# Kernel optimization log

Measured on AMD Instinct MI355X. Metric: run time of the kernel, lower is better.

Reference implementation:

```python
import jax, jax.numpy as jnp
import numpy as np

B, C, CI, T, H, W = 2, 1024, 512, 32, 14, 14
N = T * H * W


def setup_inputs() -> dict:
    key = jax.random.key(0)
    ks = jax.random.split(key, 6)
    s_in = 1.0 / np.sqrt(C)
    s_mid = 1.0 / np.sqrt(CI)
    return {
        "x": jax.random.normal(ks[0], (B, C, T, H, W), jnp.float32),
        "Wk": jax.random.normal(ks[1], (CI, C), jnp.float32) * s_in,
        "bk": jnp.zeros((CI,), jnp.float32),
        "Wq": jax.random.normal(ks[2], (CI, C), jnp.float32) * s_in,
        "bq": jnp.zeros((CI,), jnp.float32),
        "Wv": jax.random.normal(ks[3], (CI, C), jnp.float32) * s_in,
        "bv": jnp.zeros((CI,), jnp.float32),
        "Wo": jax.random.normal(ks[4], (C, CI), jnp.float32) * s_mid,
        "bo": jnp.zeros((C,), jnp.float32),
    }


def reference(x, Wk, bk, Wq, bq, Wv, bv, Wo, bo):
    # x: (B, C, T, H, W). Dropout layers are identity at inference.
    b, c, t, h, w = x.shape
    n = t * h * w
    xf = x.reshape(b, c, n)                          # (B, C, N)
    k = jnp.einsum("dc,bcn->bdn", Wk, xf) + bk[None, :, None]   # (B, CI, N)
    q = jnp.einsum("dc,bcn->bdn", Wq, xf) + bq[None, :, None]   # (B, CI, N)
    v = jnp.einsum("dc,bcn->bdn", Wv, xf) + bv[None, :, None]   # (B, CI, N)
    # alpha[b,i,j] = sum_d key[b,i,d] * query[b,d,j], scaled by 1/T
    alpha = jnp.einsum("bdi,bdj->bij", k, q) / float(t)          # (B, N, N)
    alpha = jax.nn.softmax(alpha, axis=-1)
    # y (B, CI, N) with y[b,c,i] = sum_j alpha[b,i,j] * v[b,c,j]
    y = jnp.einsum("bij,bcj->bci", alpha, v)
    out = jnp.einsum("dc,bcn->bdn", Wo, y) + bo[None, :, None]   # (B, C, N)
    return out.reshape(b, c, t, h, w) + x
```

## Files before the change

kernel.cpp:

```cpp
#include <hip/hip_runtime.h>

#define Bb 2
#define Cc 1024
#define CIi 512
#define Nn 6272
#define JH 3136
#define SCALE (1.0f / 32.0f)

typedef __bf16 bf16;
typedef __bf16 bf16x8 __attribute__((ext_vector_type(8)));
typedef __bf16 bf16x4 __attribute__((ext_vector_type(4)));
typedef float f32x4 __attribute__((ext_vector_type(4)));
typedef float f32x2 __attribute__((ext_vector_type(2)));
typedef unsigned int u32;
typedef unsigned int u32x4 __attribute__((ext_vector_type(4)));

__device__ __forceinline__ void g2l16(const void* g, void* l) {
  __builtin_amdgcn_global_load_lds(
      (const __attribute__((address_space(1))) u32*)g,
      (__attribute__((address_space(3))) u32*)(size_t)l, 16, 0, 0);
}

__global__ __launch_bounds__(256) void xpose_kernel(const float* __restrict__ x,
                                                    bf16* __restrict__ xT) {
  __shared__ float tile[32][33];
  int b = blockIdx.z;
  int n0 = blockIdx.x * 32, c0 = blockIdx.y * 32;
  int tn = threadIdx.x & 31, tr = threadIdx.x >> 5;
  const float* xp = x + ((size_t)b * Cc + c0) * Nn + n0;
  for (int i = 0; i < 4; i++) {
    int c = tr + i * 8;
    tile[c][tn] = xp[(size_t)c * Nn + tn];
  }
  __syncthreads();
  bf16* op = xT + ((size_t)b * Nn + n0) * Cc + c0;
  for (int i = 0; i < 4; i++) {
    int n = tr + i * 8;
    op[(size_t)n * Cc + tn] = (bf16)tile[tn][n];
  }
}

__global__ __launch_bounds__(256) void proj_kernel(
    const bf16* __restrict__ xT, const float* __restrict__ Wk,
    const float* __restrict__ Wq, const float* __restrict__ Wv,
    const float* __restrict__ bk, const float* __restrict__ bq,
    const float* __restrict__ bv, bf16* __restrict__ kT, bf16* __restrict__ qT,
    bf16* __restrict__ vv) {
  int z = blockIdx.z;
  int b = z / 3, proj = z % 3;
  const float* W = proj == 0 ? Wk : (proj == 1 ? Wq : Wv);
  const float* bias = proj == 0 ? bk : (proj == 1 ? bq : bv);
  int m0 = blockIdx.x * 128;
  int d0 = blockIdx.y * 128;
  __shared__ __align__(16) bf16 la[128 * 40];
  __shared__ __align__(16) bf16 lb[128 * 40];
  int tid = threadIdx.x;
  int wave = tid >> 6, lane = tid & 63, quad = lane >> 4, l16 = lane & 15;
  int wm = (wave >> 1) * 64, wn = (wave & 1) * 64;
  int row2 = tid >> 1, half = tid & 1;

  f32x4 acc[4][4] = {};
  const bf16* aSrc = xT + ((size_t)b * Nn + m0) * Cc;
  const float* bSrc = W + (size_t)(d0 + row2) * Cc;

  for (int k0 = 0; k0 < Cc; k0 += 32) {
    const u32x4* ga = (const u32x4*)(aSrc + (size_t)row2 * Cc + k0 + half * 16);
    u32x4 a0 = ga[0], a1 = ga[1];
    const f32x4* gb = (const f32x4*)(bSrc + k0 + half * 16);
    f32x4 w0 = gb[0], w1 = gb[1], w2 = gb[2], w3 = gb[3];
    *(u32x4*)&la[row2 * 40 + half * 16] = a0;
    *(u32x4*)&la[row2 * 40 + half * 16 + 8] = a1;
    bf16x8 p0 = {(bf16)w0[0], (bf16)w0[1], (bf16)w0[2], (bf16)w0[3],
                 (bf16)w1[0], (bf16)w1[1], (bf16)w1[2], (bf16)w1[3]};
    bf16x8 p1 = {(bf16)w2[0], (bf16)w2[1], (bf16)w2[2], (bf16)w2[3],
                 (bf16)w3[0], (bf16)w3[1], (bf16)w3[2], (bf16)w3[3]};
    *(bf16x8*)&lb[row2 * 40 + half * 16] = p0;
    *(bf16x8*)&lb[row2 * 40 + half * 16 + 8] = p1;
    __syncthreads();
    bf16x8 af[4], bfr[4];
    for (int t = 0; t < 4; t++)
      af[t] = *(const bf16x8*)&la[(wm + t * 16 + l16) * 40 + quad * 8];
    for (int t = 0; t < 4; t++)
      bfr[t] = *(const bf16x8*)&lb[(wn + t * 16 + l16) * 40 + quad * 8];
    for (int tm = 0; tm < 4; tm++)
      for (int tn = 0; tn < 4; tn++)
        acc[tm][tn] = __builtin_amdgcn_mfma_f32_16x16x32_bf16(
            af[tm], bfr[tn], acc[tm][tn], 0, 0, 0);
    __syncthreads();
  }
  for (int tn = 0; tn < 4; tn++) {
    int dcol = d0 + wn + tn * 16 + l16;
    float bval = bias[dcol];
    for (int tm = 0; tm < 4; tm++) {
      int nbase = m0 + wm + tm * 16 + quad * 4;
      for (int r = 0; r < 4; r++) {
        float val = acc[tm][tn][r] + bval;
        int nrow = nbase + r;
        if (proj == 0) {
          kT[((size_t)b * Nn + nrow) * CIi + dcol] = (bf16)val;
        } else if (proj == 1) {
          int ch = (dcol >> 3) ^ (nrow & 7);
          qT[((size_t)b * Nn + nrow) * CIi + ch * 8 + (dcol & 7)] = (bf16)val;
        } else {
          vv[((size_t)b * CIi + dcol) * Nn + nrow] = (bf16)val;
        }
      }
    }
  }
}

__global__ __launch_bounds__(512, 2) void attn_kernel(
    const bf16* __restrict__ kT, const bf16* __restrict__ qTs,
    const bf16* __restrict__ vv, bf16* __restrict__ yp,
    float* __restrict__ ml) {
  int l = blockIdx.x;
  int jh = l & 1, b = (l >> 1) & 1;
  int i0 = (l >> 2) * 128;
  int tid = threadIdx.x;
  int wave = tid >> 6, lane = tid & 63, quad = lane >> 4, l16 = lane & 15;
  int dw = wave * 64;

  __shared__ __align__(16) bf16 lq[2][32 * 512];
  __shared__ __align__(16) bf16 Psm[128 * 36];
  __shared__ float red[128];

  const bf16* qb = qTs + ((size_t)b * Nn + (size_t)jh * JH) * CIi;
  const bf16* vb = vv + (size_t)b * CIi * Nn + (size_t)jh * JH;

  bf16x8 kf[16];
  {
    const bf16* kp =
        kT + ((size_t)b * Nn + i0 + wave * 16 + l16) * CIi + quad * 8;
#pragma unroll
    for (int kk = 0; kk < 16; kk++) kf[kk] = *(const bf16x8*)(kp + kk * 32);
  }
  f32x4 oacc[8][4] = {};
  f32x4 l_acc = {};

  {
    const bf16* qrow = qb + (size_t)(wave * 4) * CIi + lane * 8;
#pragma unroll
    for (int r = 0; r < 4; r++)
      g2l16(qrow + (size_t)r * CIi, &lq[0][(wave * 4 + r) * 512]);
  }
  __syncthreads();

  int x0 = l16 & 7;
  for (int j0 = 0; j0 < JH; j0 += 32) {
    int t = (j0 >> 5) & 1;
    if (j0 + 32 < JH) {
      const bf16* qrow = qb + (size_t)(j0 + 32 + wave * 4) * CIi + lane * 8;
#pragma unroll
      for (int r = 0; r < 4; r++)
        g2l16(qrow + (size_t)r * CIi, &lq[t ^ 1][(wave * 4 + r) * 512]);
    }
    f32x4 s0 = {}, s1 = {};
    {
      const bf16* q0 = &lq[t][l16 * 512];
      const bf16* q1 = &lq[t][(16 + l16) * 512];
#pragma unroll
      for (int kk = 0; kk < 16; kk++) {
        int ch = (((kk * 4 + quad) ^ x0)) * 8;
        bf16x8 qf0 = *(const bf16x8*)(q0 + ch);
        bf16x8 qf1 = *(const bf16x8*)(q1 + ch);
        s0 = __builtin_amdgcn_mfma_f32_16x16x32_bf16(kf[kk], qf0, s0, 0, 0, 0);
        s1 = __builtin_amdgcn_mfma_f32_16x16x32_bf16(kf[kk], qf1, s1, 0, 0, 0);
      }
    }
    {
#pragma unroll
      for (int r = 0; r < 4; r++) {
        float p0 = __expf(fminf(fmaf(s0[r], SCALE, -2.0f), 20.0f));
        float p1 = __expf(fminf(fmaf(s1[r], SCALE, -2.0f), 20.0f));
        l_acc[r] += p0 + p1;
        int gi = wave * 16 + quad * 4 + r;
        Psm[gi * 36 + l16] = (bf16)p0;
        Psm[gi * 36 + 16 + l16] = (bf16)p1;
      }
    }
    __syncthreads();

    {
      u32x4 vf[4];
#pragma unroll
      for (int ds = 0; ds < 4; ds++)
        vf[ds] = *(const u32x4*)(vb + (size_t)(dw + ds * 16 + l16) * Nn + j0 +
                                 quad * 8);
#pragma unroll
      for (int is = 0; is < 8; is++) {
        bf16x8 pf = *(const bf16x8*)&Psm[(is * 16 + l16) * 36 + quad * 8];
#pragma unroll
        for (int ds = 0; ds < 4; ds++)
          oacc[is][ds] = __builtin_amdgcn_mfma_f32_16x16x32_bf16(
              pf, __builtin_bit_cast(bf16x8, vf[ds]), oacc[is][ds], 0, 0, 0);
      }
    }
    __syncthreads();
  }

#pragma unroll
  for (int o = 1; o < 16; o <<= 1)
#pragma unroll
    for (int r = 0; r < 4; r++) l_acc[r] += __shfl_xor(l_acc[r], o);
  if (l16 == 0) {
#pragma unroll
    for (int r = 0; r < 4; r++) {
      int gi = wave * 16 + quad * 4 + r;
      ml[(size_t)(jh * Bb + b) * Nn + i0 + gi] = l_acc[r];
      red[gi] = 1.0f / l_acc[r];
    }
  }
  __syncthreads();
  bf16* ypb = yp + ((size_t)jh * Bb + b) * Nn * CIi;
#pragma unroll
  for (int is = 0; is < 8; is++) {
    f32x4 inv = *(const f32x4*)&red[is * 16 + quad * 4];
#pragma unroll
    for (int ds = 0; ds < 4; ds++)
#pragma unroll
      for (int r = 0; r < 4; r++)
        ypb[(size_t)(i0 + is * 16 + quad * 4 + r) * CIi + dw + ds * 16 + l16] =
            (bf16)(oacc[is][ds][r] * inv[r]);
  }
}

__global__ __launch_bounds__(256) void merge_kernel(const bf16* __restrict__ yp,
                                                    const float* __restrict__ ml,
                                                    bf16* __restrict__ y) {
  int idx = blockIdx.x * 256 + threadIdx.x;
  int row = idx >> 6, c = idx & 63;
  float l0 = ml[row];
  float l1 = ml[(size_t)Bb * Nn + row];
  float inv = 1.0f / (l0 + l1);
  float w0 = l0 * inv, w1 = l1 * inv;
  bf16x8 v0 = *(const bf16x8*)&yp[(size_t)row * CIi + c * 8];
  bf16x8 v1 =
      *(const bf16x8*)&yp[(size_t)Bb * Nn * CIi + (size_t)row * CIi + c * 8];
  bf16x8 o;
#pragma unroll
  for (int k = 0; k < 8; k++)
    o[k] = (bf16)(w0 * (float)v0[k] + w1 * (float)v1[k]);
  *(bf16x8*)&y[(size_t)row * CIi + c * 8] = o;
}

__global__ __launch_bounds__(256) void out_kernel(
    const bf16* __restrict__ y, const float* __restrict__ Wo,
    const float* __restrict__ bo, const float* __restrict__ x,
    float* __restrict__ out) {
  int b = blockIdx.z;
  int d0 = blockIdx.x * 128;
  int m0 = blockIdx.y * 128;
  __shared__ __align__(16) bf16 la[128 * 40];
  __shared__ __align__(16) bf16 lb[128 * 40];
  int tid = threadIdx.x;
  int wave = tid >> 6, lane = tid & 63, quad = lane >> 4, l16 = lane & 15;
  int wm = (wave >> 1) * 64, wn = (wave & 1) * 64;
  int row2 = tid >> 1, half = tid & 1;
  f32x4 acc[4][4] = {};
  const float* aSrc = Wo + (size_t)(d0 + row2) * CIi;
  const bf16* bSrc = y + ((size_t)b * Nn + m0 + row2) * CIi;
  for (int k0 = 0; k0 < CIi; k0 += 32) {
    const f32x4* ga = (const f32x4*)(aSrc + k0 + half * 16);
    f32x4 w0 = ga[0], w1 = ga[1], w2 = ga[2], w3 = ga[3];
    const u32x4* gb = (const u32x4*)(bSrc + k0 + half * 16);
    u32x4 b0 = gb[0], b1 = gb[1];
    bf16x8 p0 = {(bf16)w0[0], (bf16)w0[1], (bf16)w0[2], (bf16)w0[3],
                 (bf16)w1[0], (bf16)w1[1], (bf16)w1[2], (bf16)w1[3]};
    bf16x8 p1 = {(bf16)w2[0], (bf16)w2[1], (bf16)w2[2], (bf16)w2[3],
                 (bf16)w3[0], (bf16)w3[1], (bf16)w3[2], (bf16)w3[3]};
    *(bf16x8*)&la[row2 * 40 + half * 16] = p0;
    *(bf16x8*)&la[row2 * 40 + half * 16 + 8] = p1;
    *(u32x4*)&lb[row2 * 40 + half * 16] = b0;
    *(u32x4*)&lb[row2 * 40 + half * 16 + 8] = b1;
    __syncthreads();
    bf16x8 af[4], bfr[4];
    for (int t = 0; t < 4; t++)
      af[t] = *(const bf16x8*)&la[(wm + t * 16 + l16) * 40 + quad * 8];
    for (int t = 0; t < 4; t++)
      bfr[t] = *(const bf16x8*)&lb[(wn + t * 16 + l16) * 40 + quad * 8];
    for (int tm = 0; tm < 4; tm++)
      for (int tn = 0; tn < 4; tn++)
        acc[tm][tn] = __builtin_amdgcn_mfma_f32_16x16x32_bf16(
            af[tm], bfr[tn], acc[tm][tn], 0, 0, 0);
    __syncthreads();
  }
  for (int tm = 0; tm < 4; tm++) {
    for (int r = 0; r < 4; r++) {
      int drow = d0 + wm + tm * 16 + quad * 4 + r;
      float bval = bo[drow];
      const float* xrow = x + ((size_t)b * Cc + drow) * Nn;
      float* orow = out + ((size_t)b * Cc + drow) * Nn;
      for (int tn = 0; tn < 4; tn++) {
        int ncol = m0 + wn + tn * 16 + l16;
        orow[ncol] = acc[tm][tn][r] + bval + xrow[ncol];
      }
    }
  }
}

extern "C" void kernel_launch(void* const* d_in, const int* in_sizes, int n_in,
                              void* d_out, int out_size, void* d_ws,
                              size_t ws_size, hipStream_t stream) {
  (void)in_sizes;
  (void)n_in;
  (void)out_size;
  (void)ws_size;
  const float* x = (const float*)d_in[0];
  const float* Wk = (const float*)d_in[1];
  const float* bk = (const float*)d_in[2];
  const float* Wq = (const float*)d_in[3];
  const float* bq = (const float*)d_in[4];
  const float* Wv = (const float*)d_in[5];
  const float* bv = (const float*)d_in[6];
  const float* Wo = (const float*)d_in[7];
  const float* bo = (const float*)d_in[8];
  float* out = (float*)d_out;

  bf16* xT = (bf16*)d_ws;
  bf16* yp = (bf16*)d_ws;
  bf16* y = (bf16*)d_ws + (size_t)Bb * Nn * Cc;
  bf16* kT = (bf16*)d_out;
  bf16* qT = kT + (size_t)Bb * Nn * CIi;
  bf16* vv = qT + (size_t)Bb * Nn * CIi;
  float* ml = (float*)((char*)d_out + (size_t)40 * 1024 * 1024);

  xpose_kernel<<<dim3(Nn / 32, Cc / 32, Bb), 256, 0, stream>>>(x, xT);
  proj_kernel<<<dim3(Nn / 128, CIi / 128, 3 * Bb), 256, 0, stream>>>(
      xT, Wk, Wq, Wv, bk, bq, bv, kT, qT, vv);
  attn_kernel<<<dim3((Nn / 128) * 2 * Bb), 512, 0, stream>>>(kT, qT, vv, yp,
                                                             ml);
  merge_kernel<<<dim3(Bb * Nn * 64 / 256), 256, 0, stream>>>(yp, ml, y);
  out_kernel<<<dim3(Cc / 128, Nn / 128, Bb), 256, 0, stream>>>(y, Wo, bo, x,
                                                               out);
}
```

Before: 577.6 us.

## Widen attention j-tile to 64 with 2D wave split of QK^T

```diff
diff --git a/kernel.cpp b/kernel.cpp
--- a/kernel.cpp
+++ b/kernel.cpp
@@ -118,81 +118,100 @@
   int i0 = (l >> 2) * 128;
   int tid = threadIdx.x;
   int wave = tid >> 6, lane = tid & 63, quad = lane >> 4, l16 = lane & 15;
+  int wi = wave & 3, wj = wave >> 2;
   int dw = wave * 64;
 
-  __shared__ __align__(16) bf16 lq[2][32 * 512];
-  __shared__ __align__(16) bf16 Psm[128 * 36];
-  __shared__ float red[128];
+  __shared__ __align__(16) bf16 lq[2][64 * 512];
+  __shared__ __align__(16) bf16 Psm[128 * 64];
+  __shared__ __align__(16) float redw[2][128];
+  __shared__ __align__(16) float redi[128];
 
   const bf16* qb = qTs + ((size_t)b * Nn + (size_t)jh * JH) * CIi;
   const bf16* vb = vv + (size_t)b * CIi * Nn + (size_t)jh * JH;
 
-  bf16x8 kf[16];
+  bf16x8 kf[2][16];
   {
     const bf16* kp =
-        kT + ((size_t)b * Nn + i0 + wave * 16 + l16) * CIi + quad * 8;
-#pragma unroll
-    for (int kk = 0; kk < 16; kk++) kf[kk] = *(const bf16x8*)(kp + kk * 32);
+        kT + ((size_t)b * Nn + i0 + wi * 32 + l16) * CIi + quad * 8;
+#pragma unroll
+    for (int h = 0; h < 2; h++)
+#pragma unroll
+      for (int kk = 0; kk < 16; kk++)
+        kf[h][kk] = *(const bf16x8*)(kp + (size_t)(h * 16) * CIi + kk * 32);
   }
   f32x4 oacc[8][4] = {};
-  f32x4 l_acc = {};
+  f32x4 l_acc[2] = {};
 
   {
-    const bf16* qrow = qb + (size_t)(wave * 4) * CIi + lane * 8;
-#pragma unroll
-    for (int r = 0; r < 4; r++)
-      g2l16(qrow + (size_t)r * CIi, &lq[0][(wave * 4 + r) * 512]);
+    const bf16* qrow = qb + (size_t)(wave * 8) * CIi + lane * 8;
+#pragma unroll
+    for (int r = 0; r < 8; r++)
+      g2l16(qrow + (size_t)r * CIi, &lq[0][(wave * 8 + r) * 512]);
   }
   __syncthreads();
 
   int x0 = l16 & 7;
-  for (int j0 = 0; j0 < JH; j0 += 32) {
-    int t = (j0 >> 5) & 1;
-    if (j0 + 32 < JH) {
-      const bf16* qrow = qb + (size_t)(j0 + 32 + wave * 4) * CIi + lane * 8;
-#pragma unroll
-      for (int r = 0; r < 4; r++)
-        g2l16(qrow + (size_t)r * CIi, &lq[t ^ 1][(wave * 4 + r) * 512]);
-    }
-    f32x4 s0 = {}, s1 = {};
+  for (int j0 = 0; j0 < JH; j0 += 64) {
+    int t = (j0 >> 6) & 1;
+    u32x4 vf[2][4];
+#pragma unroll
+    for (int jc = 0; jc < 2; jc++)
+#pragma unroll
+      for (int ds = 0; ds < 4; ds++)
+        vf[jc][ds] = *(const u32x4*)(vb + (size_t)(dw + ds * 16 + l16) * Nn +
+                                     j0 + jc * 32 + quad * 8);
+    if (j0 + 64 < JH) {
+      const bf16* qrow = qb + (size_t)(j0 + 64 + wave * 8) * CIi + lane * 8;
+#pragma unroll
+      for (int r = 0; r < 8; r++)
+        g2l16(qrow + (size_t)r * CIi, &lq[t ^ 1][(wave * 8 + r) * 512]);
+    }
+    f32x4 s[2][2] = {};
     {
-      const bf16* q0 = &lq[t][l16 * 512];
-      const bf16* q1 = &lq[t][(16 + l16) * 512];
+      const bf16* q0 = &lq[t][(wj * 32 + l16) * 512];
+      const bf16* q1 = &lq[t][(wj * 32 + 16 + l16) * 512];
 #pragma unroll
       for (int kk = 0; kk < 16; kk++) {
-        int ch = (((kk * 4 + quad) ^ x0)) * 8;
+        int ch = ((kk * 4 + quad) ^ x0) * 8;
         bf16x8 qf0 = *(const bf16x8*)(q0 + ch);
         bf16x8 qf1 = *(const bf16x8*)(q1 + ch);
-        s0 = __builtin_amdgcn_mfma_f32_16x16x32_bf16(kf[kk], qf0, s0, 0, 0, 0);
-        s1 = __builtin_amdgcn_mfma_f32_16x16x32_bf16(kf[kk], qf1, s1, 0, 0, 0);
+        s[0][0] = __builtin_amdgcn_mfma_f32_16x16x32_bf16(kf[0][kk], qf0,
+                                                          s[0][0], 0, 0, 0);
+        s[0][1] = __builtin_amdgcn_mfma_f32_16x16x32_bf16(kf[0][kk], qf1,
+                                                          s[0][1], 0, 0, 0);
+        s[1][0] = __builtin_amdgcn_mfma_f32_16x16x32_bf16(kf[1][kk], qf0,
+                                                          s[1][0], 0, 0, 0);
+        s[1][1] = __builtin_amdgcn_mfma_f32_16x16x32_bf16(kf[1][kk], qf1,
+                                                          s[1][1], 0, 0, 0);
       }
     }
-    {
-#pragma unroll
-      for (int r = 0; r < 4; r++) {
-        float p0 = __expf(fminf(fmaf(s0[r], SCALE, -2.0f), 20.0f));
-        float p1 = __expf(fminf(fmaf(s1[r], SCALE, -2.0f), 20.0f));
-        l_acc[r] += p0 + p1;
-        int gi = wave * 16 + quad * 4 + r;
-        Psm[gi * 36 + l16] = (bf16)p0;
-        Psm[gi * 36 + 16 + l16] = (bf16)p1;
-      }
-    }
-    __syncthreads();
-
-    {
-      u32x4 vf[4];
-#pragma unroll
-      for (int ds = 0; ds < 4; ds++)
-        vf[ds] = *(const u32x4*)(vb + (size_t)(dw + ds * 16 + l16) * Nn + j0 +
-                                 quad * 8);
-#pragma unroll
-      for (int is = 0; is < 8; is++) {
-        bf16x8 pf = *(const bf16x8*)&Psm[(is * 16 + l16) * 36 + quad * 8];
+#pragma unroll
+    for (int h = 0; h < 2; h++)
+#pragma unroll
+      for (int jb = 0; jb < 2; jb++)
+#pragma unroll
+        for (int r = 0; r < 4; r++) {
+          float p = __expf(fminf(fmaf(s[h][jb][r], SCALE, -2.0f), 20.0f));
+          l_acc[h][r] += p;
+          int gi = wi * 32 + h * 16 + quad * 4 + r;
+          int gj = wj * 32 + jb * 16 + l16;
+          Psm[gi * 64 + (((gj >> 3) ^ (gi & 7)) << 3) + (gj & 7)] = (bf16)p;
+        }
+    asm volatile("s_waitcnt lgkmcnt(0)" ::: "memory");
+    __builtin_amdgcn_s_barrier();
+    asm volatile("" ::: "memory");
+
+#pragma unroll
+    for (int is = 0; is < 8; is++) {
+#pragma unroll
+      for (int jc = 0; jc < 2; jc++) {
+        bf16x8 pf = *(const bf16x8*)&Psm[(is * 16 + l16) * 64 +
+                                         (((jc * 4 + quad) ^ x0) << 3)];
 #pragma unroll
         for (int ds = 0; ds < 4; ds++)
           oacc[is][ds] = __builtin_amdgcn_mfma_f32_16x16x32_bf16(
-              pf, __builtin_bit_cast(bf16x8, vf[ds]), oacc[is][ds], 0, 0, 0);
+              pf, __builtin_bit_cast(bf16x8, vf[jc][ds]), oacc[is][ds], 0, 0,
+              0);
       }
     }
     __syncthreads();
@@ -201,20 +220,27 @@
 #pragma unroll
   for (int o = 1; o < 16; o <<= 1)
 #pragma unroll
-    for (int r = 0; r < 4; r++) l_acc[r] += __shfl_xor(l_acc[r], o);
+    for (int h = 0; h < 2; h++)
+#pragma unroll
+      for (int r = 0; r < 4; r++) l_acc[h][r] += __shfl_xor(l_acc[h][r], o);
   if (l16 == 0) {
 #pragma unroll
-    for (int r = 0; r < 4; r++) {
-      int gi = wave * 16 + quad * 4 + r;
-      ml[(size_t)(jh * Bb + b) * Nn + i0 + gi] = l_acc[r];
-      red[gi] = 1.0f / l_acc[r];
-    }
+    for (int h = 0; h < 2; h++)
+#pragma unroll
+      for (int r = 0; r < 4; r++)
+        redw[wj][wi * 32 + h * 16 + quad * 4 + r] = l_acc[h][r];
+  }
+  __syncthreads();
+  if (tid < 128) {
+    float s = redw[0][tid] + redw[1][tid];
+    ml[(size_t)(jh * Bb + b) * Nn + i0 + tid] = s;
+    redi[tid] = 1.0f / s;
   }
   __syncthreads();
   bf16* ypb = yp + ((size_t)jh * Bb + b) * Nn * CIi;
 #pragma unroll
   for (int is = 0; is < 8; is++) {
-    f32x4 inv = *(const f32x4*)&red[is * 16 + quad * 4];
+    f32x4 inv = *(const f32x4*)&redi[is * 16 + quad * 4];
 #pragma unroll
     for (int ds = 0; ds < 4; ds++)
 #pragma unroll
```

Result: slower. 1.054 ms (+82.4%).
